# Optimization experiments

Measured on AMD Instinct MI355X. Metric: run time of the kernel, lower is better.

## Reference

```python
import jax, jax.numpy as jnp
import numpy as np

B, C, T, F, D, S = 16, 128, 64, 128, 2, 62  # batch, w_dim, seq_in, feat, dilation, seq_out


def setup_inputs() -> dict:
    key = jax.random.key(0)
    ks = jax.random.split(key, 9)
    x = jax.random.normal(ks[0], (B, C, T, F), dtype=jnp.float32)
    # depthwise (2,1) dilated conv params: weight[c, tap]
    w_tanh = jax.random.normal(ks[1], (C, 2), dtype=jnp.float32) * 0.5
    b_tanh = jax.random.normal(ks[2], (C,), dtype=jnp.float32) * 0.1
    w_sig = jax.random.normal(ks[3], (C, 2), dtype=jnp.float32) * 0.5
    b_sig = jax.random.normal(ks[4], (C,), dtype=jnp.float32) * 0.1
    # depthwise 1x1 out conv: one scalar weight + bias per channel
    w_out = jax.random.normal(ks[5], (C,), dtype=jnp.float32) * 0.5
    b_out = jax.random.normal(ks[6], (C,), dtype=jnp.float32) * 0.1
    # residual Linear(seq_in=T -> seq_out=S)
    w_res = jax.random.normal(ks[7], (S, T), dtype=jnp.float32) * (1.0 / np.sqrt(T))
    b_res = jax.random.normal(ks[8], (S,), dtype=jnp.float32) * 0.1
    return {"x": x, "w_tanh": w_tanh, "b_tanh": b_tanh, "w_sig": w_sig,
            "b_sig": b_sig, "w_out": w_out, "b_out": b_out,
            "w_res": w_res, "b_res": b_res, "dilation": D}


def reference(x, w_tanh, b_tanh, w_sig, b_sig, w_out, b_out, w_res, b_res, dilation):
    d = dilation
    # depthwise dilated conv, kernel (2,1): out[t] = w[0]*x[t] + w[1]*x[t+d]
    x0 = x[:, :, : x.shape[2] - d, :]          # [B,C,S,F]
    x1 = x[:, :, d:, :]                         # [B,C,S,F]
    cexp = lambda v: v[None, :, None, None]
    xt = x0 * cexp(w_tanh[:, 0]) + x1 * cexp(w_tanh[:, 1]) + cexp(b_tanh)
    xs = x0 * cexp(w_sig[:, 0]) + x1 * cexp(w_sig[:, 1]) + cexp(b_sig)
    gate = jnp.tanh(xt) * jax.nn.sigmoid(xs)    # [B,C,S,F]
    # residual: Linear over T, output laid out as [B,C,S,F]
    res = jnp.einsum('bctf,st->bcsf', x, w_res) + b_res[None, None, :, None]
    # depthwise 1x1 conv
    out = (gate + res) * cexp(w_out) + cexp(b_out)
    return out
```

## Files before the change

### kernel.cpp

```cpp
#include <hip/hip_runtime.h>


typedef __attribute__((ext_vector_type(8)))  short short8;
typedef __attribute__((ext_vector_type(4)))  float f32x4;
typedef __attribute__((ext_vector_type(4)))  int   i32x4;
typedef __attribute__((ext_vector_type(2)))  int   i32x2;

constexpr int Bc = 16, Cc = 128, Tc = 64, Fc = 128, Sc = 62, DIL = 2;
constexpr int LDSTW    = 72;
constexpr int XT_BYTES = Fc * LDSTW * 2;
constexpr int A_BYTES  = 8 * 64 * 16;
constexpr int LDS_TOT  = XT_BYTES + A_BYTES;

__device__ inline unsigned cvt_pk_bf16(float lo, float hi) {
    unsigned r;
    asm("v_cvt_pk_bf16_f32 %0, %1, %2" : "=v"(r) : "v"(lo), "v"(hi));
    return r;
}

__device__ inline float bf16_lo(int u) { return __uint_as_float(((unsigned)u) << 16); }
__device__ inline float bf16_hi(int u) { return __uint_as_float(((unsigned)u) & 0xFFFF0000u); }

__global__ __launch_bounds__(256, 5)
void gated_mfma_kernel(const float* __restrict__ x,
                       const float* __restrict__ w_tanh,
                       const float* __restrict__ b_tanh,
                       const float* __restrict__ w_sig,
                       const float* __restrict__ b_sig,
                       const float* __restrict__ w_out,
                       const float* __restrict__ b_out,
                       const float* __restrict__ w_res,
                       const float* __restrict__ b_res,
                       float* __restrict__ out)
{
    __shared__ i32x4 smem[LDS_TOT / 16];
    char* lds_base = (char*)smem;
    char* lds_a    = lds_base + XT_BYTES;

    const int bc   = blockIdx.x;
    const int c    = bc & (Cc - 1);
    const int tid  = threadIdx.x;
    const int lane = tid & 63;
    const int w    = tid >> 6;
    const int g    = lane >> 4;
    const int r16  = lane & 15;

    const float wt0 = w_tanh[2 * c + 0], wt1 = w_tanh[2 * c + 1], bt = b_tanh[c];
    const float ws0 = w_sig[2 * c + 0],  ws1 = w_sig[2 * c + 1],  bs = b_sig[c];
    const float wo  = w_out[c],          bo  = b_out[c];

    const int fq = tid & 31;
    const int tg = tid >> 5;
    const float* xp = x + (size_t)bc * (Tc * Fc);
    f32x4 v[8];
#pragma unroll
    for (int u = 0; u < 8; ++u)
        v[u] = *(const f32x4*)(xp + (8 * tg + u) * Fc + 4 * fq);

#pragma unroll
    for (int i = 0; i < 2; ++i) {
        const int u   = tid + 256 * i;
        const int row = u >> 3;
        const int k8  = u & 7;
        f32x4 a0 = f32x4{0.f, 0.f, 0.f, 0.f};
        f32x4 a1 = f32x4{0.f, 0.f, 0.f, 0.f};
        if (row < Sc) {
            const float* wr = w_res + row * Tc + 8 * k8;
            a0 = *(const f32x4*)(wr);
            a1 = *(const f32x4*)(wr + 4);
        }
        const unsigned p0 = cvt_pk_bf16(a0.x, a0.y);
        const unsigned p1 = cvt_pk_bf16(a0.z, a0.w);
        const unsigned p2 = cvt_pk_bf16(a1.x, a1.y);
        const unsigned p3 = cvt_pk_bf16(a1.z, a1.w);
        const int slot = ((row >> 4) * 2 + (k8 >> 2)) * 64 + (k8 & 3) * 16 + (row & 15);
        *(i32x4*)(lds_a + slot * 16) = i32x4{(int)p0, (int)p1, (int)p2, (int)p3};
    }

    const int tsw = 8 * (tg ^ (fq & 3));
#pragma unroll
    for (int fj = 0; fj < 4; ++fj) {
        const unsigned p0 = cvt_pk_bf16(v[0][fj], v[1][fj]);
        const unsigned p1 = cvt_pk_bf16(v[2][fj], v[3][fj]);
        const unsigned p2 = cvt_pk_bf16(v[4][fj], v[5][fj]);
        const unsigned p3 = cvt_pk_bf16(v[6][fj], v[7][fj]);
        *(i32x4*)(lds_base + ((4 * fq + fj) * LDSTW + tsw) * 2) =
            i32x4{(int)p0, (int)p1, (int)p2, (int)p3};
    }

    f32x4 acc[4][2];
#pragma unroll
    for (int rt = 0; rt < 4; ++rt) {
        f32x4 bv;
#pragma unroll
        for (int j = 0; j < 4; ++j) {
            const int idx = 16 * rt + 4 * g + j;
            bv[j] = b_res[idx < Sc ? idx : Sc - 1];
        }
        acc[rt][0] = bv;
        acc[rt][1] = bv;
    }

    __syncthreads();

    short8 A[4][2];
#pragma unroll
    for (int rt = 0; rt < 4; ++rt)
#pragma unroll
        for (int kt = 0; kt < 2; ++kt)
            A[rt][kt] = *(const short8*)(lds_a + ((rt * 2 + kt) * 64 + lane) * 16);

    const int col0 = 32 * w + r16;
    const int swz8 = 8 * (g ^ (r16 >> 2));
#pragma unroll
    for (int kt = 0; kt < 2; ++kt) {
        short8 Bf[2];
#pragma unroll
        for (int ct = 0; ct < 2; ++ct)
            Bf[ct] = *(const short8*)(lds_base +
                        ((col0 + 16 * ct) * LDSTW + 32 * kt + swz8) * 2);
#pragma unroll
        for (int rt = 0; rt < 4; ++rt)
#pragma unroll
            for (int ct = 0; ct < 2; ++ct)
                acc[rt][ct] = __builtin_amdgcn_mfma_f32_16x16x32_bf16(
                    A[rt][kt], Bf[ct], acc[rt][ct], 0, 0, 0);
    }

    const int sw8 = 8 * (r16 >> 2);
    float* op = out + (size_t)bc * (Sc * Fc);
#pragma unroll
    for (int rt = 0; rt < 4; ++rt) {
        const int r0 = 16 * rt + 4 * g;
#pragma unroll
        for (int ct = 0; ct < 2; ++ct) {
            const int col = col0 + 16 * ct;
            const i32x2 d1 = *(const i32x2*)(lds_base + (col * LDSTW + (r0 ^ sw8)) * 2);
            const i32x2 d2 = *(const i32x2*)(lds_base + (col * LDSTW + ((r0 + 4) ^ sw8)) * 2);
            const float t0 = bf16_lo(d1.x);
            const float t1 = bf16_hi(d1.x);
            const float t2 = bf16_lo(d1.y);
            const float t3 = bf16_hi(d1.y);
            const float t4 = bf16_lo(d2.x);
            const float t5 = bf16_hi(d2.x);

#define GATE_OUT(reg, xa, xb)                                                     \
            if (r0 + (reg) < Sc) {                                                \
                const float xt  = fmaf((xa), wt0, fmaf((xb), wt1, bt));           \
                const float xsg = fmaf((xa), ws0, fmaf((xb), ws1, bs));           \
                const float e2  = __expf(2.0f * xt);                              \
                const float em  = __expf(-xsg);                                   \
                const float gate = (e2 - 1.0f) *                                  \
                    __builtin_amdgcn_rcpf((e2 + 1.0f) * (1.0f + em));             \
                op[(r0 + (reg)) * Fc + col] =                                     \
                    fmaf(gate + acc[rt][ct][reg], wo, bo);                        \
            }
            GATE_OUT(0, t0, t2)
            GATE_OUT(1, t1, t3)
            GATE_OUT(2, t2, t4)
            GATE_OUT(3, t3, t5)
#undef GATE_OUT
        }
    }
}

extern "C" void kernel_launch(void* const* d_in, const int* in_sizes, int n_in,
                              void* d_out, int out_size, void* d_ws, size_t ws_size,
                              hipStream_t stream)
{
    const float* x      = (const float*)d_in[0];
    const float* w_tanh = (const float*)d_in[1];
    const float* b_tanh = (const float*)d_in[2];
    const float* w_sig  = (const float*)d_in[3];
    const float* b_sig  = (const float*)d_in[4];
    const float* w_out  = (const float*)d_in[5];
    const float* b_out  = (const float*)d_in[6];
    const float* w_res  = (const float*)d_in[7];
    const float* b_res  = (const float*)d_in[8];

    float* out = (float*)d_out;

    gated_mfma_kernel<<<Bc * Cc, 256, 0, stream>>>(
        x, w_tanh, b_tanh, w_sig, b_sig, w_out, b_out, w_res, b_res, out);
}
```

Before: 27.55 us.

## Precompute bf16 MFMA weight fragments in a prep kernel and shrink LDS

Moves the w_res fp32-to-bf16 conversion and fragment layout out of every block into a one-block prep kernel that writes fragments and padded bias into workspace. The main kernel then loads A fragments straight from global memory (L2-cached) instead of staging them through LDS, which cuts LDS usage and lets launch bounds rise from 5 to 8 blocks per CU. The output loop is restructured per column tile to reduce live accumulator registers. It adds a second kernel launch each call and per-lane global loads of the weight fragments.

```diff
diff --git a/kernel.cpp b/kernel.cpp
--- a/kernel.cpp
+++ b/kernel.cpp
@@ -9,8 +9,6 @@
 constexpr int Bc = 16, Cc = 128, Tc = 64, Fc = 128, Sc = 62, DIL = 2;
 constexpr int LDSTW    = 72;
 constexpr int XT_BYTES = Fc * LDSTW * 2;
-constexpr int A_BYTES  = 8 * 64 * 16;
-constexpr int LDS_TOT  = XT_BYTES + A_BYTES;
 
 __device__ inline unsigned cvt_pk_bf16(float lo, float hi) {
     unsigned r;
@@ -21,7 +19,35 @@
 __device__ inline float bf16_lo(int u) { return __uint_as_float(((unsigned)u) << 16); }
 __device__ inline float bf16_hi(int u) { return __uint_as_float(((unsigned)u) & 0xFFFF0000u); }
 
-__global__ __launch_bounds__(256, 5)
+__global__ void prep_kernel(const float* __restrict__ w_res,
+                            const float* __restrict__ b_res,
+                            void* __restrict__ ws)
+{
+    const int tid = threadIdx.x;
+    i32x4* wa = (i32x4*)ws;
+    float* brs = (float*)((char*)ws + 8192);
+    for (int u = tid; u < 512; u += 256) {
+        const int frag = u >> 6, lane = u & 63;
+        const int rt = frag >> 1, kt = frag & 1;
+        const int row = 16 * rt + (lane & 15);
+        const int g = lane >> 4;
+        unsigned p[4];
+#pragma unroll
+        for (int q = 0; q < 4; ++q) {
+            float lo = 0.f, hi = 0.f;
+            if (row < Sc) {
+                const int k = 32 * kt + 8 * g + 2 * q;
+                lo = w_res[row * Tc + k];
+                hi = w_res[row * Tc + k + 1];
+            }
+            p[q] = cvt_pk_bf16(lo, hi);
+        }
+        wa[u] = i32x4{(int)p[0], (int)p[1], (int)p[2], (int)p[3]};
+    }
+    if (tid < 64) brs[tid] = (tid < Sc) ? b_res[tid] : 0.f;
+}
+
+__global__ __launch_bounds__(256, 8)
 void gated_mfma_kernel(const float* __restrict__ x,
                        const float* __restrict__ w_tanh,
                        const float* __restrict__ b_tanh,
@@ -29,13 +55,11 @@
                        const float* __restrict__ b_sig,
                        const float* __restrict__ w_out,
                        const float* __restrict__ b_out,
-                       const float* __restrict__ w_res,
-                       const float* __restrict__ b_res,
+                       const void* __restrict__ ws,
                        float* __restrict__ out)
 {
-    __shared__ i32x4 smem[LDS_TOT / 16];
+    __shared__ i32x4 smem[XT_BYTES / 16];
     char* lds_base = (char*)smem;
-    char* lds_a    = lds_base + XT_BYTES;
 
     const int bc   = blockIdx.x;
     const int c    = bc & (Cc - 1);
@@ -57,26 +81,6 @@
     for (int u = 0; u < 8; ++u)
         v[u] = *(const f32x4*)(xp + (8 * tg + u) * Fc + 4 * fq);
 
-#pragma unroll
-    for (int i = 0; i < 2; ++i) {
-        const int u   = tid + 256 * i;
-        const int row = u >> 3;
-        const int k8  = u & 7;
-        f32x4 a0 = f32x4{0.f, 0.f, 0.f, 0.f};
-        f32x4 a1 = f32x4{0.f, 0.f, 0.f, 0.f};
-        if (row < Sc) {
-            const float* wr = w_res + row * Tc + 8 * k8;
-            a0 = *(const f32x4*)(wr);
-            a1 = *(const f32x4*)(wr + 4);
-        }
-        const unsigned p0 = cvt_pk_bf16(a0.x, a0.y);
-        const unsigned p1 = cvt_pk_bf16(a0.z, a0.w);
-        const unsigned p2 = cvt_pk_bf16(a1.x, a1.y);
-        const unsigned p3 = cvt_pk_bf16(a1.z, a1.w);
-        const int slot = ((row >> 4) * 2 + (k8 >> 2)) * 64 + (k8 & 3) * 16 + (row & 15);
-        *(i32x4*)(lds_a + slot * 16) = i32x4{(int)p0, (int)p1, (int)p2, (int)p3};
-    }
-
     const int tsw = 8 * (tg ^ (fq & 3));
 #pragma unroll
     for (int fj = 0; fj < 4; ++fj) {
@@ -88,53 +92,38 @@
             i32x4{(int)p0, (int)p1, (int)p2, (int)p3};
     }
 
-    f32x4 acc[4][2];
-#pragma unroll
-    for (int rt = 0; rt < 4; ++rt) {
-        f32x4 bv;
-#pragma unroll
-        for (int j = 0; j < 4; ++j) {
-            const int idx = 16 * rt + 4 * g + j;
-            bv[j] = b_res[idx < Sc ? idx : Sc - 1];
-        }
-        acc[rt][0] = bv;
-        acc[rt][1] = bv;
-    }
-
     __syncthreads();
 
-    short8 A[4][2];
-#pragma unroll
-    for (int rt = 0; rt < 4; ++rt)
-#pragma unroll
-        for (int kt = 0; kt < 2; ++kt)
-            A[rt][kt] = *(const short8*)(lds_a + ((rt * 2 + kt) * 64 + lane) * 16);
+    const short8* wa  = (const short8*)ws;
+    const float*  brs = (const float*)((const char*)ws + 8192);
 
     const int col0 = 32 * w + r16;
     const int swz8 = 8 * (g ^ (r16 >> 2));
+    const int sw8  = 8 * (r16 >> 2);
+    float* op = out + (size_t)bc * (Sc * Fc);
+
 #pragma unroll
-    for (int kt = 0; kt < 2; ++kt) {
-        short8 Bf[2];
-#pragma unroll
-        for (int ct = 0; ct < 2; ++ct)
-            Bf[ct] = *(const short8*)(lds_base +
-                        ((col0 + 16 * ct) * LDSTW + 32 * kt + swz8) * 2);
+    for (int ct = 0; ct < 2; ++ct) {
+        const int col = col0 + 16 * ct;
+
+        f32x4 acc[4];
 #pragma unroll
         for (int rt = 0; rt < 4; ++rt)
+            acc[rt] = *(const f32x4*)(brs + 16 * rt + 4 * g);
+
 #pragma unroll
-            for (int ct = 0; ct < 2; ++ct)
-                acc[rt][ct] = __builtin_amdgcn_mfma_f32_16x16x32_bf16(
-                    A[rt][kt], Bf[ct], acc[rt][ct], 0, 0, 0);
-    }
+        for (int kt = 0; kt < 2; ++kt) {
+            const short8 Bf = *(const short8*)(lds_base +
+                                (col * LDSTW + 32 * kt + swz8) * 2);
+#pragma unroll
+            for (int rt = 0; rt < 4; ++rt)
+                acc[rt] = __builtin_amdgcn_mfma_f32_16x16x32_bf16(
+                    wa[(rt * 2 + kt) * 64 + lane], Bf, acc[rt], 0, 0, 0);
+        }
 
-    const int sw8 = 8 * (r16 >> 2);
-    float* op = out + (size_t)bc * (Sc * Fc);
 #pragma unroll
-    for (int rt = 0; rt < 4; ++rt) {
-        const int r0 = 16 * rt + 4 * g;
-#pragma unroll
-        for (int ct = 0; ct < 2; ++ct) {
-            const int col = col0 + 16 * ct;
+        for (int rt = 0; rt < 4; ++rt) {
+            const int r0 = 16 * rt + 4 * g;
             const i32x2 d1 = *(const i32x2*)(lds_base + (col * LDSTW + (r0 ^ sw8)) * 2);
             const i32x2 d2 = *(const i32x2*)(lds_base + (col * LDSTW + ((r0 + 4) ^ sw8)) * 2);
             const float t0 = bf16_lo(d1.x);
@@ -153,7 +142,7 @@
                 const float gate = (e2 - 1.0f) *                                  \
                     __builtin_amdgcn_rcpf((e2 + 1.0f) * (1.0f + em));             \
                 op[(r0 + (reg)) * Fc + col] =                                     \
-                    fmaf(gate + acc[rt][ct][reg], wo, bo);                        \
+                    fmaf(gate + acc[rt][reg], wo, bo);                            \
             }
             GATE_OUT(0, t0, t2)
             GATE_OUT(1, t1, t3)
@@ -180,6 +169,7 @@
 
     float* out = (float*)d_out;
 
+    prep_kernel<<<1, 256, 0, stream>>>(w_res, b_res, d_ws);
     gated_mfma_kernel<<<Bc * Cc, 256, 0, stream>>>(
-        x, w_tanh, b_tanh, w_sig, b_sig, w_out, b_out, w_res, b_res, out);
+        x, w_tanh, b_tanh, w_sig, b_sig, w_out, b_out, d_ws, out);
 }
```

Result: slower. 41.09 us (+49.2%).

## Process two (b,c) slices per block, prefetching the second during the first

Applied to the files above, without the earlier changes.

Each block now handles two consecutive batch-channel slices. The block reuses the bf16 w_res tile staged in LDS for both slices, and it issues the global loads of the second slice's x before running the first slice's epilogue, so load latency overlaps the gate math and stores. The grid is halved, which gives fewer blocks per CU and adds an extra barrier plus higher register pressure from holding the prefetched data.

```diff
diff --git a/kernel.cpp b/kernel.cpp
--- a/kernel.cpp
+++ b/kernel.cpp
@@ -37,131 +37,169 @@
     char* lds_base = (char*)smem;
     char* lds_a    = lds_base + XT_BYTES;
 
-    const int bc   = blockIdx.x;
-    const int c    = bc & (Cc - 1);
+    const int bc0  = blockIdx.x * 2;
+    const int bc1  = bc0 + 1;
+    const int c0   = bc0 & (Cc - 1);
+    const int c1   = bc1 & (Cc - 1);
     const int tid  = threadIdx.x;
     const int lane = tid & 63;
     const int w    = tid >> 6;
     const int g    = lane >> 4;
     const int r16  = lane & 15;
 
-    const float wt0 = w_tanh[2 * c + 0], wt1 = w_tanh[2 * c + 1], bt = b_tanh[c];
-    const float ws0 = w_sig[2 * c + 0],  ws1 = w_sig[2 * c + 1],  bs = b_sig[c];
-    const float wo  = w_out[c],          bo  = b_out[c];
-
     const int fq = tid & 31;
     const int tg = tid >> 5;
-    const float* xp = x + (size_t)bc * (Tc * Fc);
-    f32x4 v[8];
+    const int tsw  = 8 * (tg ^ (fq & 3));
+    const int col0 = 32 * w + r16;
+    const int swz8 = 8 * (g ^ (r16 >> 2));
+    const int sw8  = 8 * (r16 >> 2);
+
+    const float* xp0 = x + (size_t)bc0 * (Tc * Fc);
+    const float* xp1 = x + (size_t)bc1 * (Tc * Fc);
+
+    f32x4 acc[4][2];
+
+    auto epilogue = [&](float* op, float wt0, float wt1, float bt,
+                        float ws0, float ws1, float bs, float wo, float bo) {
+#pragma unroll
+        for (int rt = 0; rt < 4; ++rt) {
+            const int r0 = 16 * rt + 4 * g;
+#pragma unroll
+            for (int ct = 0; ct < 2; ++ct) {
+                const int col = col0 + 16 * ct;
+                const i32x2 d1 = *(const i32x2*)(lds_base + (col * LDSTW + (r0 ^ sw8)) * 2);
+                const i32x2 d2 = *(const i32x2*)(lds_base + (col * LDSTW + ((r0 + 4) ^ sw8)) * 2);
+                const float t[6] = { bf16_lo(d1.x), bf16_hi(d1.x),
+                                     bf16_lo(d1.y), bf16_hi(d1.y),
+                                     bf16_lo(d2.x), bf16_hi(d2.x) };
+#pragma unroll
+                for (int reg = 0; reg < 4; ++reg) {
+                    if (r0 + reg < Sc) {
+                        const float xa = t[reg];
+                        const float xb = t[reg + 2];
+                        const float xt  = fmaf(xa, wt0, fmaf(xb, wt1, bt));
+                        const float xsg = fmaf(xa, ws0, fmaf(xb, ws1, bs));
+                        const float e2  = __expf(2.0f * xt);
+                        const float em  = __expf(-xsg);
+                        const float gate = (e2 - 1.0f) *
+                            __builtin_amdgcn_rcpf((e2 + 1.0f) * (1.0f + em));
+                        op[(r0 + reg) * Fc + col] = fmaf(gate + acc[rt][ct][reg], wo, bo);
+                    }
+                }
+            }
+        }
+    };
+
+    auto acc_init = [&]() {
+#pragma unroll
+        for (int rt = 0; rt < 4; ++rt) {
+            f32x4 bv;
+#pragma unroll
+            for (int j = 0; j < 4; ++j) {
+                const int idx = 16 * rt + 4 * g + j;
+                bv[j] = b_res[idx < Sc ? idx : Sc - 1];
+            }
+            acc[rt][0] = bv;
+            acc[rt][1] = bv;
+        }
+    };
+
+    auto mfma_block = [&]() {
+        short8 A[4][2];
+#pragma unroll
+        for (int rt = 0; rt < 4; ++rt)
+#pragma unroll
+            for (int kt = 0; kt < 2; ++kt)
+                A[rt][kt] = *(const short8*)(lds_a + ((rt * 2 + kt) * 64 + lane) * 16);
+#pragma unroll
+        for (int kt = 0; kt < 2; ++kt) {
+            short8 Bf[2];
+#pragma unroll
+            for (int ct = 0; ct < 2; ++ct)
+                Bf[ct] = *(const short8*)(lds_base +
+                            ((col0 + 16 * ct) * LDSTW + 32 * kt + swz8) * 2);
+#pragma unroll
+            for (int rt = 0; rt < 4; ++rt)
+#pragma unroll
+                for (int ct = 0; ct < 2; ++ct)
+                    acc[rt][ct] = __builtin_amdgcn_mfma_f32_16x16x32_bf16(
+                        A[rt][kt], Bf[ct], acc[rt][ct], 0, 0, 0);
+        }
+    };
+
+    {
+        f32x4 v[8];
+#pragma unroll
+        for (int u = 0; u < 8; ++u)
+            v[u] = *(const f32x4*)(xp0 + (8 * tg + u) * Fc + 4 * fq);
+
+#pragma unroll
+        for (int i = 0; i < 2; ++i) {
+            const int u   = tid + 256 * i;
+            const int row = u >> 3;
+            const int k8  = u & 7;
+            f32x4 a0 = f32x4{0.f, 0.f, 0.f, 0.f};
+            f32x4 a1 = f32x4{0.f, 0.f, 0.f, 0.f};
+            if (row < Sc) {
+                const float* wr = w_res + row * Tc + 8 * k8;
+                a0 = *(const f32x4*)(wr);
+                a1 = *(const f32x4*)(wr + 4);
+            }
+            const unsigned p0 = cvt_pk_bf16(a0.x, a0.y);
+            const unsigned p1 = cvt_pk_bf16(a0.z, a0.w);
+            const unsigned p2 = cvt_pk_bf16(a1.x, a1.y);
+            const unsigned p3 = cvt_pk_bf16(a1.z, a1.w);
+            const int slot = ((row >> 4) * 2 + (k8 >> 2)) * 64 + (k8 & 3) * 16 + (row & 15);
+            *(i32x4*)(lds_a + slot * 16) = i32x4{(int)p0, (int)p1, (int)p2, (int)p3};
+        }
+
+#pragma unroll
+        for (int fj = 0; fj < 4; ++fj) {
+            const unsigned p0 = cvt_pk_bf16(v[0][fj], v[1][fj]);
+            const unsigned p1 = cvt_pk_bf16(v[2][fj], v[3][fj]);
+            const unsigned p2 = cvt_pk_bf16(v[4][fj], v[5][fj]);
+            const unsigned p3 = cvt_pk_bf16(v[6][fj], v[7][fj]);
+            *(i32x4*)(lds_base + ((4 * fq + fj) * LDSTW + tsw) * 2) =
+                i32x4{(int)p0, (int)p1, (int)p2, (int)p3};
+        }
+    }
+
+    acc_init();
+    __syncthreads();
+
+    mfma_block();
+
+    f32x4 v1[8];
 #pragma unroll
     for (int u = 0; u < 8; ++u)
-        v[u] = *(const f32x4*)(xp + (8 * tg + u) * Fc + 4 * fq);
-
-#pragma unroll
-    for (int i = 0; i < 2; ++i) {
-        const int u   = tid + 256 * i;
-        const int row = u >> 3;
-        const int k8  = u & 7;
-        f32x4 a0 = f32x4{0.f, 0.f, 0.f, 0.f};
-        f32x4 a1 = f32x4{0.f, 0.f, 0.f, 0.f};
-        if (row < Sc) {
-            const float* wr = w_res + row * Tc + 8 * k8;
-            a0 = *(const f32x4*)(wr);
-            a1 = *(const f32x4*)(wr + 4);
-        }
-        const unsigned p0 = cvt_pk_bf16(a0.x, a0.y);
-        const unsigned p1 = cvt_pk_bf16(a0.z, a0.w);
-        const unsigned p2 = cvt_pk_bf16(a1.x, a1.y);
-        const unsigned p3 = cvt_pk_bf16(a1.z, a1.w);
-        const int slot = ((row >> 4) * 2 + (k8 >> 2)) * 64 + (k8 & 3) * 16 + (row & 15);
-        *(i32x4*)(lds_a + slot * 16) = i32x4{(int)p0, (int)p1, (int)p2, (int)p3};
-    }
-
-    const int tsw = 8 * (tg ^ (fq & 3));
+        v1[u] = *(const f32x4*)(xp1 + (8 * tg + u) * Fc + 4 * fq);
+
+    epilogue(out + (size_t)bc0 * (Sc * Fc),
+             w_tanh[2 * c0 + 0], w_tanh[2 * c0 + 1], b_tanh[c0],
+             w_sig[2 * c0 + 0],  w_sig[2 * c0 + 1],  b_sig[c0],
+             w_out[c0], b_out[c0]);
+
+    __syncthreads();
+
 #pragma unroll
     for (int fj = 0; fj < 4; ++fj) {
-        const unsigned p0 = cvt_pk_bf16(v[0][fj], v[1][fj]);
-        const unsigned p1 = cvt_pk_bf16(v[2][fj], v[3][fj]);
-        const unsigned p2 = cvt_pk_bf16(v[4][fj], v[5][fj]);
-        const unsigned p3 = cvt_pk_bf16(v[6][fj], v[7][fj]);
+        const unsigned p0 = cvt_pk_bf16(v1[0][fj], v1[1][fj]);
+        const unsigned p1 = cvt_pk_bf16(v1[2][fj], v1[3][fj]);
+        const unsigned p2 = cvt_pk_bf16(v1[4][fj], v1[5][fj]);
+        const unsigned p3 = cvt_pk_bf16(v1[6][fj], v1[7][fj]);
         *(i32x4*)(lds_base + ((4 * fq + fj) * LDSTW + tsw) * 2) =
             i32x4{(int)p0, (int)p1, (int)p2, (int)p3};
     }
 
-    f32x4 acc[4][2];
-#pragma unroll
-    for (int rt = 0; rt < 4; ++rt) {
-        f32x4 bv;
-#pragma unroll
-        for (int j = 0; j < 4; ++j) {
-            const int idx = 16 * rt + 4 * g + j;
-            bv[j] = b_res[idx < Sc ? idx : Sc - 1];
-        }
-        acc[rt][0] = bv;
-        acc[rt][1] = bv;
-    }
-
+    acc_init();
     __syncthreads();
 
-    short8 A[4][2];
-#pragma unroll
-    for (int rt = 0; rt < 4; ++rt)
-#pragma unroll
-        for (int kt = 0; kt < 2; ++kt)
-            A[rt][kt] = *(const short8*)(lds_a + ((rt * 2 + kt) * 64 + lane) * 16);
-
-    const int col0 = 32 * w + r16;
-    const int swz8 = 8 * (g ^ (r16 >> 2));
-#pragma unroll
-    for (int kt = 0; kt < 2; ++kt) {
-        short8 Bf[2];
-#pragma unroll
-        for (int ct = 0; ct < 2; ++ct)
-            Bf[ct] = *(const short8*)(lds_base +
-                        ((col0 + 16 * ct) * LDSTW + 32 * kt + swz8) * 2);
-#pragma unroll
-        for (int rt = 0; rt < 4; ++rt)
-#pragma unroll
-            for (int ct = 0; ct < 2; ++ct)
-                acc[rt][ct] = __builtin_amdgcn_mfma_f32_16x16x32_bf16(
-                    A[rt][kt], Bf[ct], acc[rt][ct], 0, 0, 0);
-    }
-
-    const int sw8 = 8 * (r16 >> 2);
-    float* op = out + (size_t)bc * (Sc * Fc);
-#pragma unroll
-    for (int rt = 0; rt < 4; ++rt) {
-        const int r0 = 16 * rt + 4 * g;
-#pragma unroll
-        for (int ct = 0; ct < 2; ++ct) {
-            const int col = col0 + 16 * ct;
-            const i32x2 d1 = *(const i32x2*)(lds_base + (col * LDSTW + (r0 ^ sw8)) * 2);
-            const i32x2 d2 = *(const i32x2*)(lds_base + (col * LDSTW + ((r0 + 4) ^ sw8)) * 2);
-            const float t0 = bf16_lo(d1.x);
-            const float t1 = bf16_hi(d1.x);
-            const float t2 = bf16_lo(d1.y);
-            const float t3 = bf16_hi(d1.y);
-            const float t4 = bf16_lo(d2.x);
-            const float t5 = bf16_hi(d2.x);
-
-#define GATE_OUT(reg, xa, xb)                                                     \
-            if (r0 + (reg) < Sc) {                                                \
-                const float xt  = fmaf((xa), wt0, fmaf((xb), wt1, bt));           \
-                const float xsg = fmaf((xa), ws0, fmaf((xb), ws1, bs));           \
-                const float e2  = __expf(2.0f * xt);                              \
-                const float em  = __expf(-xsg);                                   \
-                const float gate = (e2 - 1.0f) *                                  \
-                    __builtin_amdgcn_rcpf((e2 + 1.0f) * (1.0f + em));             \
-                op[(r0 + (reg)) * Fc + col] =                                     \
-                    fmaf(gate + acc[rt][ct][reg], wo, bo);                        \
-            }
-            GATE_OUT(0, t0, t2)
-            GATE_OUT(1, t1, t3)
-            GATE_OUT(2, t2, t4)
-            GATE_OUT(3, t3, t5)
-#undef GATE_OUT
-        }
-    }
+    mfma_block();
+
+    epilogue(out + (size_t)bc1 * (Sc * Fc),
+             w_tanh[2 * c1 + 0], w_tanh[2 * c1 + 1], b_tanh[c1],
+             w_sig[2 * c1 + 0],  w_sig[2 * c1 + 1],  b_sig[c1],
+             w_out[c1], b_out[c1]);
 }
 
 extern "C" void kernel_launch(void* const* d_in, const int* in_sizes, int n_in,
@@ -180,6 +218,6 @@
 
     float* out = (float*)d_out;
 
-    gated_mfma_kernel<<<Bc * Cc, 256, 0, stream>>>(
+    gated_mfma_kernel<<<(Bc * Cc) / 2, 256, 0, stream>>>(
         x, w_tanh, b_tanh, w_sig, b_sig, w_out, b_out, w_res, b_res, out);
 }
```

Result: slower. 31.91 us (+15.8%).
